# Optimization experiments

Hardware: AMD Instinct MI355X
Metric: run time of the kernel (lower is better)

Reference implementation:

```python
import jax, jax.numpy as jnp
import numpy as np

EPS = 8.0 / 255.0  # hparams['epsilon']


def setup_inputs() -> dict:
    key = jax.random.key(0)
    k1, k2, k3, k4 = jax.random.split(key, 4)
    B, N, C, H, Wd, K = 128, 96, 3, 32, 32, 10
    D = C * H * Wd
    imgs = jax.random.uniform(k1, (B, C, H, Wd), dtype=jnp.float32)
    # sample_deltas: uniform in [-eps, eps]
    deltas = 2.0 * EPS * jax.random.uniform(k2, (N, B, C, H, Wd), dtype=jnp.float32) - EPS
    W = jax.random.normal(k3, (D, K), dtype=jnp.float32) * (1.0 / np.sqrt(D))
    b = jnp.zeros((K,), dtype=jnp.float32)
    labels = jax.random.randint(k4, (B,), 0, K, dtype=jnp.int32)
    ind = 91  # math.ceil(N * proportion) - 1 with N=96, proportion=0.95
    return {"imgs": imgs, "deltas": deltas, "W": W, "b": b, "labels": labels, "ind": ind}


def reference(imgs, deltas, W, b, labels, ind):
    N, B = deltas.shape[:2]
    # pert_imgs = clamp(imgs + delta, 0, 1), flattened for the linear classifier
    x = jnp.clip(imgs[None] + deltas, 0.0, 1.0).reshape(N, B, -1)  # [N,B,D]
    logits = jnp.einsum('nbd,dk->nbk', x, W) + b                    # [N,B,K]
    logp = jax.nn.log_softmax(logits, axis=-1)
    # pert_loss1 = CE(logits, labels), per-sample
    loss1 = -jnp.take_along_axis(logp, labels[None, :, None], axis=-1)[..., 0]  # [N,B]
    # top-2 labels; new_labels = second-best class
    _, top2 = jax.lax.top_k(logits, 2)
    top1, second = top2[..., 0], top2[..., 1]
    loss2 = -jnp.take_along_axis(logp, second[..., None], axis=-1)[..., 0]      # [N,B]
    # mask: if argmax != label, pert_loss2[i] = -10000
    loss2 = jnp.where(top1 == labels[None, :], loss2, jnp.float32(-10000.0))
    # layout [B,N] as in torch.cat(..., dim=1)
    l1 = loss1.T
    l2 = loss2.T
    order = jnp.argsort(l1 - l2, axis=1)                 # sort(loss1 - loss2) indices
    sel_idx = order[:, ind]                              # per-sample selected column
    # torch.tensor(list) detaches -> no gradient through selected losses
    selected = jax.lax.stop_gradient(jnp.take_along_axis(l2, sel_idx[:, None], axis=1))  # [B,1]
    robust_loss = jnp.mean(jnp.mean(l1 - selected, axis=1))
    return robust_loss
```

## Files before the change

kernel.cpp:

```cpp
#include <hip/hip_runtime.h>
#include <math.h>

#define BB 128
#define NN 96
#define DD 3072
#define KK 10
#define G  4

__global__ __launch_bounds__(256) void k1_logits(
    const float* __restrict__ imgs,
    const float* __restrict__ deltas,
    const float* __restrict__ W,
    const float* __restrict__ bias,
    const int*   __restrict__ labels,
    float* __restrict__ l1_ws,
    float* __restrict__ l2_ws)
{
    const int lane = threadIdx.x & 63;
    const int task = blockIdx.x * 4 + (threadIdx.x >> 6);
    const int b    = task & 127;
    const int n0   = (task >> 7) * G;

    float acc[G][KK];
#pragma unroll
    for (int j = 0; j < G; ++j)
#pragma unroll
        for (int k = 0; k < KK; ++k) acc[j][k] = 0.f;

    for (int c = 0; c < 12; ++c) {
        const int i0 = c * 256 + lane * 4;
        float w[40];
        const float4* wp = (const float4*)(W + (size_t)i0 * KK);
#pragma unroll
        for (int m = 0; m < 10; ++m) {
            float4 v = wp[m];
            w[4*m+0] = v.x; w[4*m+1] = v.y; w[4*m+2] = v.z; w[4*m+3] = v.w;
        }
        const float4 im = *(const float4*)(imgs + (size_t)b * DD + i0);
#pragma unroll
        for (int j = 0; j < G; ++j) {
            const int n = n0 + j;
            const float4 dl = *(const float4*)(deltas + ((size_t)(n * BB + b)) * DD + i0);
            const float x0 = fminf(fmaxf(im.x + dl.x, 0.f), 1.f);
            const float x1 = fminf(fmaxf(im.y + dl.y, 0.f), 1.f);
            const float x2 = fminf(fmaxf(im.z + dl.z, 0.f), 1.f);
            const float x3 = fminf(fmaxf(im.w + dl.w, 0.f), 1.f);
#pragma unroll
            for (int k = 0; k < KK; ++k) {
                acc[j][k] = fmaf(x3, w[30+k],
                            fmaf(x2, w[20+k],
                            fmaf(x1, w[10+k],
                            fmaf(x0, w[k], acc[j][k]))));
            }
        }
    }

#pragma unroll
    for (int j = 0; j < G; ++j)
#pragma unroll
        for (int k = 0; k < KK; ++k) {
            float s = acc[j][k];
#pragma unroll
            for (int off = 1; off < 64; off <<= 1)
                s += __shfl_xor(s, off, 64);
            acc[j][k] = s;
        }

    if (lane < G) {
        float lg[KK];
#pragma unroll
        for (int k = 0; k < KK; ++k) {
            float v = acc[0][k];
            if (lane == 1) v = acc[1][k];
            if (lane == 2) v = acc[2][k];
            if (lane == 3) v = acc[3][k];
            lg[k] = v + bias[k];
        }
        const int n = n0 + lane;
        int top1 = 0; float m1 = lg[0];
#pragma unroll
        for (int k = 1; k < KK; ++k) if (lg[k] > m1) { m1 = lg[k]; top1 = k; }
        int sec = (top1 == 0) ? 1 : 0; float m2 = lg[sec];
#pragma unroll
        for (int k = 0; k < KK; ++k)
            if (k != top1 && lg[k] > m2) { m2 = lg[k]; sec = k; }
        float se = 0.f;
#pragma unroll
        for (int k = 0; k < KK; ++k) se += expf(lg[k] - m1);
        const float lse = m1 + logf(se);
        const int lab = labels[b];
        const float loss1 = lse - lg[lab];
        const float loss2 = (top1 == lab) ? (lse - lg[sec]) : -10000.0f;
        l1_ws[b * NN + n] = loss1;
        l2_ws[b * NN + n] = loss2;
    }
}

__global__ __launch_bounds__(128) void k2_select(
    const float* __restrict__ l1_ws, const float* __restrict__ l2_ws,
    const int* __restrict__ ind_p, float* __restrict__ perb)
{
    const int b = blockIdx.x;
    const int t = threadIdx.x;
    __shared__ float sd[NN];
    __shared__ float sl2[NN];
    __shared__ float ssel;
    __shared__ float swsum[2];

    float myl1 = 0.f, myd = 0.f;
    if (t < NN) {
        const float a = l1_ws[b * NN + t];
        const float c = l2_ws[b * NN + t];
        myl1 = a; myd = a - c;
        sd[t] = myd; sl2[t] = c;
    }
    __syncthreads();

    if (t < NN) {
        int rank = 0;
        for (int j = 0; j < NN; ++j) {
            const float dj = sd[j];
            rank += (dj < myd) || (dj == myd && j < t);
        }
        if (rank == ind_p[0]) ssel = sl2[t];
    }

    float s = myl1;
#pragma unroll
    for (int off = 32; off >= 1; off >>= 1) s += __shfl_down(s, off, 64);
    if ((t & 63) == 0) swsum[t >> 6] = s;
    __syncthreads();
    if (t == 0) {
        const float total = swsum[0] + swsum[1];
        perb[b] = total / 96.0f - ssel;
    }
}

__global__ __launch_bounds__(128) void k3_final(
    const float* __restrict__ perb, float* __restrict__ out)
{
    const int t = threadIdx.x;
    float s = perb[t];
#pragma unroll
    for (int off = 32; off >= 1; off >>= 1) s += __shfl_down(s, off, 64);
    __shared__ float sw[2];
    if ((t & 63) == 0) sw[t >> 6] = s;
    __syncthreads();
    if (t == 0) out[0] = (sw[0] + sw[1]) / 128.0f;
}

extern "C" void kernel_launch(void* const* d_in, const int* in_sizes, int n_in,
                              void* d_out, int out_size, void* d_ws, size_t ws_size,
                              hipStream_t stream) {
    const float* imgs   = (const float*)d_in[0];
    const float* deltas = (const float*)d_in[1];
    const float* W      = (const float*)d_in[2];
    const float* bias   = (const float*)d_in[3];
    const int*   labels = (const int*)d_in[4];
    const int*   ind    = (const int*)d_in[5];
    float* out = (float*)d_out;

    float* l1_ws = (float*)d_ws;
    float* l2_ws = l1_ws + NN * BB;
    float* perb  = l2_ws + NN * BB;

    k1_logits<<<dim3(768), dim3(256), 0, stream>>>(
        imgs, deltas, W, bias, labels, l1_ws, l2_ws);
    k2_select<<<dim3(BB), dim3(128), 0, stream>>>(l1_ws, l2_ws, ind, perb);
    k3_final<<<dim3(1), dim3(128), 0, stream>>>(perb, out);
}
```

Before: 265.2 us.

## Compute logits with bf16 MFMA tiles and pre-packed bf16 weights

```diff
diff --git a/kernel.cpp b/kernel.cpp
--- a/kernel.cpp
+++ b/kernel.cpp
@@ -1,82 +1,96 @@
 #include <hip/hip_runtime.h>
+#include <hip/hip_bf16.h>
 #include <math.h>
 
 #define BB 128
 #define NN 96
 #define DD 3072
 #define KK 10
-#define G  4
+#define SPL 8
+#define KST 12
 
-__global__ __launch_bounds__(256) void k1_logits(
+typedef short s16x8 __attribute__((ext_vector_type(8)));
+typedef float f32x4 __attribute__((ext_vector_type(4)));
+
+__global__ __launch_bounds__(256) void k0_pack(
+    const float* __restrict__ W, unsigned short* __restrict__ pwg)
+{
+    const int r = blockIdx.x * 256 + threadIdx.x;
+    const int col  = r & 15;
+    const int quad = (r >> 4) & 3;
+    const int kb   = r >> 6;
+    union { unsigned short us[8]; uint4 v; } rec;
+#pragma unroll
+    for (int j = 0; j < 8; ++j) {
+        const int k = kb * 32 + quad * 8 + j;
+        const float v = (col < KK) ? W[k * KK + col] : 0.0f;
+        const __hip_bfloat16 h = __float2bfloat16(v);
+        __builtin_memcpy(&rec.us[j], &h, 2);
+    }
+    ((uint4*)pwg)[r] = rec.v;
+}
+
+__global__ __launch_bounds__(512) void k1_mfma(
     const float* __restrict__ imgs,
     const float* __restrict__ deltas,
-    const float* __restrict__ W,
+    const unsigned short* __restrict__ pwg,
     const float* __restrict__ bias,
     const int*   __restrict__ labels,
     float* __restrict__ l1_ws,
     float* __restrict__ l2_ws)
 {
     const int lane = threadIdx.x & 63;
-    const int task = blockIdx.x * 4 + (threadIdx.x >> 6);
-    const int b    = task & 127;
-    const int n0   = (task >> 7) * G;
+    const int wv   = threadIdx.x >> 6;
+    const int tile = blockIdx.x;
+    const int r0   = tile * 16;
+    const int n    = r0 >> 7;
+    const int b0   = r0 & 127;
+    const int m    = lane & 15;
+    const int quad = lane >> 4;
 
-    float acc[G][KK];
+    const float* ap = deltas + (size_t)(r0 + m) * DD + wv * (KST * 32) + quad * 8;
+    const float* ip = imgs   + (size_t)(b0 + m) * DD + wv * (KST * 32) + quad * 8;
+    const unsigned short* wp = pwg + ((size_t)(wv * KST) * 64 + lane) * 8;
+
+    f32x4 acc = {0.f, 0.f, 0.f, 0.f};
+#pragma unroll 2
+    for (int s = 0; s < KST; ++s) {
+        const float4 d0 = *(const float4*)(ap);
+        const float4 d1 = *(const float4*)(ap + 4);
+        const float4 i0 = *(const float4*)(ip);
+        const float4 i1 = *(const float4*)(ip + 4);
+        const s16x8 bfrag = *(const s16x8*)(wp);
+        float x[8];
+        x[0] = d0.x + i0.x; x[1] = d0.y + i0.y; x[2] = d0.z + i0.z; x[3] = d0.w + i0.w;
+        x[4] = d1.x + i1.x; x[5] = d1.y + i1.y; x[6] = d1.z + i1.z; x[7] = d1.w + i1.w;
+        s16x8 afrag;
 #pragma unroll
-    for (int j = 0; j < G; ++j)
-#pragma unroll
-        for (int k = 0; k < KK; ++k) acc[j][k] = 0.f;
-
-    for (int c = 0; c < 12; ++c) {
-        const int i0 = c * 256 + lane * 4;
-        float w[40];
-        const float4* wp = (const float4*)(W + (size_t)i0 * KK);
-#pragma unroll
-        for (int m = 0; m < 10; ++m) {
-            float4 v = wp[m];
-            w[4*m+0] = v.x; w[4*m+1] = v.y; w[4*m+2] = v.z; w[4*m+3] = v.w;
+        for (int j = 0; j < 8; ++j) {
+            const float xc = fminf(fmaxf(x[j], 0.f), 1.f);
+            const __hip_bfloat16 h = __float2bfloat16(xc);
+            unsigned short us; __builtin_memcpy(&us, &h, 2);
+            afrag[j] = (short)us;
         }
-        const float4 im = *(const float4*)(imgs + (size_t)b * DD + i0);
-#pragma unroll
-        for (int j = 0; j < G; ++j) {
-            const int n = n0 + j;
-            const float4 dl = *(const float4*)(deltas + ((size_t)(n * BB + b)) * DD + i0);
-            const float x0 = fminf(fmaxf(im.x + dl.x, 0.f), 1.f);
-            const float x1 = fminf(fmaxf(im.y + dl.y, 0.f), 1.f);
-            const float x2 = fminf(fmaxf(im.z + dl.z, 0.f), 1.f);
-            const float x3 = fminf(fmaxf(im.w + dl.w, 0.f), 1.f);
-#pragma unroll
-            for (int k = 0; k < KK; ++k) {
-                acc[j][k] = fmaf(x3, w[30+k],
-                            fmaf(x2, w[20+k],
-                            fmaf(x1, w[10+k],
-                            fmaf(x0, w[k], acc[j][k]))));
-            }
-        }
+        acc = __builtin_amdgcn_mfma_f32_16x16x32_bf16(afrag, bfrag, acc, 0, 0, 0);
+        ap += 32; ip += 32; wp += 512;
     }
 
+    __shared__ float sred[SPL][16][16];
 #pragma unroll
-    for (int j = 0; j < G; ++j)
-#pragma unroll
-        for (int k = 0; k < KK; ++k) {
-            float s = acc[j][k];
-#pragma unroll
-            for (int off = 1; off < 64; off <<= 1)
-                s += __shfl_xor(s, off, 64);
-            acc[j][k] = s;
-        }
+    for (int reg = 0; reg < 4; ++reg)
+        sred[wv][quad * 4 + reg][m] = acc[reg];
+    __syncthreads();
 
-    if (lane < G) {
+    if (wv == 0 && lane < 16) {
+        const int rr = lane;
         float lg[KK];
 #pragma unroll
         for (int k = 0; k < KK; ++k) {
-            float v = acc[0][k];
-            if (lane == 1) v = acc[1][k];
-            if (lane == 2) v = acc[2][k];
-            if (lane == 3) v = acc[3][k];
-            lg[k] = v + bias[k];
+            float s = 0.f;
+#pragma unroll
+            for (int sp = 0; sp < SPL; ++sp) s += sred[sp][rr][k];
+            lg[k] = s + bias[k];
         }
-        const int n = n0 + lane;
         int top1 = 0; float m1 = lg[0];
 #pragma unroll
         for (int k = 1; k < KK; ++k) if (lg[k] > m1) { m1 = lg[k]; top1 = k; }
@@ -88,6 +102,7 @@
 #pragma unroll
         for (int k = 0; k < KK; ++k) se += expf(lg[k] - m1);
         const float lse = m1 + logf(se);
+        const int b = b0 + rr;
         const int lab = labels[b];
         const float loss1 = lse - lg[lab];
         const float loss2 = (top1 == lab) ? (lse - lg[sec]) : -10000.0f;
@@ -163,9 +178,11 @@
     float* l1_ws = (float*)d_ws;
     float* l2_ws = l1_ws + NN * BB;
     float* perb  = l2_ws + NN * BB;
+    unsigned short* pwg = (unsigned short*)(perb + BB);
 
-    k1_logits<<<dim3(768), dim3(256), 0, stream>>>(
-        imgs, deltas, W, bias, labels, l1_ws, l2_ws);
+    k0_pack<<<dim3(24), dim3(256), 0, stream>>>(W, pwg);
+    k1_mfma<<<dim3(768), dim3(512), 0, stream>>>(
+        imgs, deltas, pwg, bias, labels, l1_ws, l2_ws);
     k2_select<<<dim3(BB), dim3(128), 0, stream>>>(l1_ws, l2_ws, ind, perb);
     k3_final<<<dim3(1), dim3(128), 0, stream>>>(perb, out);
 }
```

Result: faster. 238.8 us (-10.0%).
